# Kernel tuning notes

Measured on AMD Instinct MI355X. Metric: run time of the kernel, lower is better.

The kernel has to match this reference:

```python
import jax, jax.numpy as jnp
import numpy as np

N_NODES = 100000
HEADS = 4
NEG_SLOPE = 0.2


def setup_inputs() -> dict:
    key = jax.random.key(0)
    ks = jax.random.split(key, 16)
    in_dim, hidden, emb = 128, 64, 64
    hc = hidden // HEADS  # per-head channels layer1
    ec = emb // HEADS     # per-head channels layer2

    def glorot(k, shape):
        fan = shape[0] + shape[-1]
        lim = jnp.sqrt(6.0 / fan)
        return jax.random.uniform(k, shape, jnp.float32, -lim, lim)

    x = jax.random.normal(ks[0], (N_NODES, in_dim), jnp.float32)
    edge_index = jax.random.randint(ks[1], (2, 1600000), 0, N_NODES, jnp.int64)
    return {
        "x": x,
        "edge_index": edge_index,
        "W1": glorot(ks[2], (in_dim, hidden)),
        "a1_src": glorot(ks[3], (HEADS, hc)),
        "a1_dst": glorot(ks[4], (HEADS, hc)),
        "b1": jnp.zeros((hidden,), jnp.float32),
        "W2": glorot(ks[5], (hidden, emb)),
        "a2_src": glorot(ks[6], (HEADS, ec)),
        "a2_dst": glorot(ks[7], (HEADS, ec)),
        "b2": jnp.zeros((emb,), jnp.float32),
        "Wp": glorot(ks[8], (emb, emb)),
        "bp": jnp.zeros((emb,), jnp.float32),
    }


def gat_layer(x, src, dst, W, a_src, a_dst, b):
    """PyG GATConv (concat=True, add_self_loops already in src/dst, no dropout/eval)."""
    N = x.shape[0]
    H, C = a_src.shape
    xw = (x @ W).reshape(N, H, C)                       # [N,H,C]
    al_src = jnp.einsum('nhc,hc->nh', xw, a_src)        # [N,H]
    al_dst = jnp.einsum('nhc,hc->nh', xw, a_dst)
    e = al_src[src] + al_dst[dst]                       # [E,H]
    e = jnp.where(e > 0, e, NEG_SLOPE * e)              # leaky_relu
    # segment softmax over incoming edges of each destination node
    m = jax.ops.segment_max(e, dst, num_segments=N)     # [N,H]
    m = jnp.where(jnp.isfinite(m), m, 0.0)
    ee = jnp.exp(e - m[dst])
    s = jax.ops.segment_sum(ee, dst, num_segments=N)    # [N,H]
    alpha = ee / (s[dst] + 1e-16)                       # [E,H]
    msg = xw[src] * alpha[:, :, None]                   # [E,H,C]
    out = jax.ops.segment_sum(msg, dst, num_segments=N) # [N,H,C]
    return out.reshape(N, H * C) + b


def reference(x, edge_index, W1, a1_src, a1_dst, b1, W2, a2_src, a2_dst, b2, Wp, bp):
    N = x.shape[0]
    loops = jnp.arange(N, dtype=edge_index.dtype)
    src = jnp.concatenate([edge_index[0], loops])
    dst = jnp.concatenate([edge_index[1], loops])
    h = jax.nn.elu(gat_layer(x, src, dst, W1, a1_src, a1_dst, b1))
    h = gat_layer(h, src, dst, W2, a2_src, a2_dst, b2)
    return jax.nn.elu(h) @ Wp + bp
```

## Files before the change

### kernel.cpp

```cpp
#include <hip/hip_runtime.h>
#include <hip/hip_bf16.h>
#include <math.h>

#define NEG_SLOPE 0.2f
#define BCAP 6144
#define ECHUNK 8192

typedef __bf16 bf16x8 __attribute__((ext_vector_type(8)));
typedef float  f32x4  __attribute__((ext_vector_type(4)));

__device__ __forceinline__ unsigned short f2b(float f) {
    union { float f; unsigned u; } c; c.f = f;
    unsigned r = (c.u + 0x7fffu + ((c.u >> 16) & 1u)) >> 16;
    return (unsigned short)r;
}
__device__ __forceinline__ float b2f(unsigned short s) {
    union { unsigned u; float f; } c; c.u = ((unsigned)s) << 16;
    return c.f;
}

__global__ __launch_bounds__(256) void k_feat1(
    const float* __restrict__ x, const float* __restrict__ W1,
    const float* __restrict__ a_src, const float* __restrict__ a_dst,
    unsigned short* __restrict__ xwb, float* __restrict__ als, float* __restrict__ ald,
    int* __restrict__ bcur, int NB, int N)
{
    int t = threadIdx.x;
    int gid = blockIdx.x * 256 + t;
    if (gid < NB) bcur[gid] = 0;

    __shared__ unsigned short WT[64][136];
    for (int f = t; f < 128 * 64; f += 256) {
        int k = f >> 6, c = f & 63;
        WT[c][k] = f2b(W1[f]);
    }
    __syncthreads();
    int wave = t >> 6, lane = t & 63;
    int lrow = lane & 15, lgrp = lane >> 4;
    int r0 = blockIdx.x * 64 + wave * 16;
    if (r0 >= N) return;

    bf16x8 bf[4][4];
#pragma unroll
    for (int ct = 0; ct < 4; ++ct)
#pragma unroll
        for (int ks = 0; ks < 4; ++ks)
            bf[ct][ks] = *(const bf16x8*)&WT[ct * 16 + lrow][ks * 32 + lgrp * 8];

    f32x4 acc[4];
#pragma unroll
    for (int ct = 0; ct < 4; ++ct) acc[ct] = (f32x4){0.f, 0.f, 0.f, 0.f};

    int rowA = r0 + lrow; if (rowA >= N) rowA = N - 1;
    const float* xp = x + (size_t)rowA * 128 + lgrp * 8;
#pragma unroll
    for (int ks = 0; ks < 4; ++ks) {
        f32x4 v0 = *(const f32x4*)(xp + ks * 32);
        f32x4 v1 = *(const f32x4*)(xp + ks * 32 + 4);
        union { unsigned short s[8]; bf16x8 b; } af;
        af.s[0] = f2b(v0[0]); af.s[1] = f2b(v0[1]); af.s[2] = f2b(v0[2]); af.s[3] = f2b(v0[3]);
        af.s[4] = f2b(v1[0]); af.s[5] = f2b(v1[1]); af.s[6] = f2b(v1[2]); af.s[7] = f2b(v1[3]);
#pragma unroll
        for (int ct = 0; ct < 4; ++ct)
            acc[ct] = __builtin_amdgcn_mfma_f32_16x16x32_bf16(af.b, bf[ct][ks], acc[ct], 0, 0, 0);
    }

    float asv[4], adv[4];
#pragma unroll
    for (int ct = 0; ct < 4; ++ct) { asv[ct] = a_src[ct * 16 + lrow]; adv[ct] = a_dst[ct * 16 + lrow]; }
#pragma unroll
    for (int q = 0; q < 4; ++q) {
        int row = r0 + lgrp * 4 + q;
        bool ok = row < N;
#pragma unroll
        for (int ct = 0; ct < 4; ++ct) {
            float v = acc[ct][q];
            if (ok) xwb[(size_t)row * 64 + ct * 16 + lrow] = f2b(v);
            float ps = v * asv[ct], pd = v * adv[ct];
#pragma unroll
            for (int m = 1; m < 16; m <<= 1) {
                ps += __shfl_xor(ps, m, 64);
                pd += __shfl_xor(pd, m, 64);
            }
            if (ok && lrow == 0) { als[row * 4 + ct] = ps; ald[row * 4 + ct] = pd; }
        }
    }
}

__global__ __launch_bounds__(256) void k_feat2(
    const unsigned short* __restrict__ hb, const float* __restrict__ W,
    const float* __restrict__ a_src, const float* __restrict__ a_dst,
    unsigned short* __restrict__ xwb, float* __restrict__ als, float* __restrict__ ald, int N)
{
    __shared__ unsigned short WT[64][72];
    int t = threadIdx.x;
    for (int f = t; f < 64 * 64; f += 256) {
        int k = f >> 6, c = f & 63;
        WT[c][k] = f2b(W[f]);
    }
    __syncthreads();
    int wave = t >> 6, lane = t & 63;
    int lrow = lane & 15, lgrp = lane >> 4;
    int r0 = blockIdx.x * 64 + wave * 16;
    if (r0 >= N) return;

    bf16x8 bf[4][2];
#pragma unroll
    for (int ct = 0; ct < 4; ++ct)
#pragma unroll
        for (int ks = 0; ks < 2; ++ks)
            bf[ct][ks] = *(const bf16x8*)&WT[ct * 16 + lrow][ks * 32 + lgrp * 8];

    f32x4 acc[4];
#pragma unroll
    for (int ct = 0; ct < 4; ++ct) acc[ct] = (f32x4){0.f, 0.f, 0.f, 0.f};

    int rowA = r0 + lrow; if (rowA >= N) rowA = N - 1;
    const unsigned short* hp = hb + (size_t)rowA * 64 + lgrp * 8;
#pragma unroll
    for (int ks = 0; ks < 2; ++ks) {
        bf16x8 af = *(const bf16x8*)(hp + ks * 32);
#pragma unroll
        for (int ct = 0; ct < 4; ++ct)
            acc[ct] = __builtin_amdgcn_mfma_f32_16x16x32_bf16(af, bf[ct][ks], acc[ct], 0, 0, 0);
    }

    float asv[4], adv[4];
#pragma unroll
    for (int ct = 0; ct < 4; ++ct) { asv[ct] = a_src[ct * 16 + lrow]; adv[ct] = a_dst[ct * 16 + lrow]; }
#pragma unroll
    for (int q = 0; q < 4; ++q) {
        int row = r0 + lgrp * 4 + q;
        bool ok = row < N;
#pragma unroll
        for (int ct = 0; ct < 4; ++ct) {
            float v = acc[ct][q];
            if (ok) xwb[(size_t)row * 64 + ct * 16 + lrow] = f2b(v);
            float ps = v * asv[ct], pd = v * adv[ct];
#pragma unroll
            for (int m = 1; m < 16; m <<= 1) {
                ps += __shfl_xor(ps, m, 64);
                pd += __shfl_xor(pd, m, 64);
            }
            if (ok && lrow == 0) { als[row * 4 + ct] = ps; ald[row * 4 + ct] = pd; }
        }
    }
}

__global__ __launch_bounds__(256) void k_proj(
    const unsigned short* __restrict__ gb, const float* __restrict__ Wp,
    const float* __restrict__ bp, float* __restrict__ out, int N)
{
    __shared__ unsigned short WT[64][72];
    int t = threadIdx.x;
    for (int f = t; f < 64 * 64; f += 256) {
        int k = f >> 6, c = f & 63;
        WT[c][k] = f2b(Wp[f]);
    }
    __syncthreads();
    int wave = t >> 6, lane = t & 63;
    int lrow = lane & 15, lgrp = lane >> 4;
    int r0 = blockIdx.x * 64 + wave * 16;
    if (r0 >= N) return;

    bf16x8 bf[4][2];
#pragma unroll
    for (int ct = 0; ct < 4; ++ct)
#pragma unroll
        for (int ks = 0; ks < 2; ++ks)
            bf[ct][ks] = *(const bf16x8*)&WT[ct * 16 + lrow][ks * 32 + lgrp * 8];

    f32x4 acc[4];
#pragma unroll
    for (int ct = 0; ct < 4; ++ct) acc[ct] = (f32x4){0.f, 0.f, 0.f, 0.f};

    int rowA = r0 + lrow; if (rowA >= N) rowA = N - 1;
    const unsigned short* gp = gb + (size_t)rowA * 64 + lgrp * 8;
#pragma unroll
    for (int ks = 0; ks < 2; ++ks) {
        bf16x8 af = *(const bf16x8*)(gp + ks * 32);
#pragma unroll
        for (int ct = 0; ct < 4; ++ct)
            acc[ct] = __builtin_amdgcn_mfma_f32_16x16x32_bf16(af, bf[ct][ks], acc[ct], 0, 0, 0);
    }

    float bpv[4];
#pragma unroll
    for (int ct = 0; ct < 4; ++ct) bpv[ct] = bp[ct * 16 + lrow];
#pragma unroll
    for (int q = 0; q < 4; ++q) {
        int row = r0 + lgrp * 4 + q;
        if (row >= N) break;
#pragma unroll
        for (int ct = 0; ct < 4; ++ct)
            out[(size_t)row * 64 + ct * 16 + lrow] = acc[ct][q] + bpv[ct];
    }
}

__global__ __launch_bounds__(256) void k_bucket(const int* __restrict__ src, const int* __restrict__ dst,
                                                int* __restrict__ bcur, unsigned* __restrict__ bbuf,
                                                int E, int NB) {
    __shared__ int cnt[512];
    __shared__ int base[512];
    int t = threadIdx.x;
    int e0 = blockIdx.x * ECHUNK;
    int e1 = e0 + ECHUNK; if (e1 > E) e1 = E;
    for (int i = t; i < NB; i += 256) cnt[i] = 0;
    __syncthreads();
    for (int i = e0 + t; i < e1; i += 256) atomicAdd(&cnt[dst[i] >> 8], 1);
    __syncthreads();
    for (int i = t; i < NB; i += 256) {
        int c = cnt[i];
        base[i] = c ? atomicAdd(&bcur[i], c) : 0;
        cnt[i] = 0;
    }
    __syncthreads();
    for (int i = e0 + t; i < e1; i += 256) {
        int d = dst[i];
        int b = d >> 8;
        int rel = atomicAdd(&cnt[b], 1);
        int pos = base[b] + rel;
        if (pos < BCAP)
            bbuf[(size_t)b * BCAP + pos] = ((unsigned)src[i] << 8) | (unsigned)(d & 255);
    }
}

__global__ __launch_bounds__(512) void k_scanbases(const int* __restrict__ bcur, int* __restrict__ bbase,
                                                   int NB, int N) {
    __shared__ int ts[512];
    int t = threadIdx.x;
    int v = 0;
    if (t < NB) {
        int nb = bcur[t]; if (nb > BCAP) nb = BCAP;
        int vn = N - t * 256; if (vn > 256) vn = 256; if (vn < 0) vn = 0;
        v = nb + vn;
    }
    ts[t] = v;
    __syncthreads();
    for (int off = 1; off < 512; off <<= 1) {
        int u = (t >= off) ? ts[t - off] : 0;
        __syncthreads();
        ts[t] += u;
        __syncthreads();
    }
    if (t < NB) bbase[t] = ts[t] - v;
}

__global__ __launch_bounds__(256) void k_csr(const int* __restrict__ bcur, const unsigned* __restrict__ bbuf,
                                             const int* __restrict__ bbase,
                                             int* __restrict__ offs, int* __restrict__ ssrc, int N) {
    __shared__ unsigned ebuf[BCAP];
    __shared__ int cnt[256];
    __shared__ int scn[256];
    int t = threadIdx.x, b = blockIdx.x;
    int node = b * 256 + t;
    int nb = bcur[b]; if (nb > BCAP) nb = BCAP;
    const unsigned* bp = bbuf + (size_t)b * BCAP;
    cnt[t] = (node < N) ? 1 : 0;
    __syncthreads();
    for (int j = t; j < nb; j += 256) {
        unsigned v = bp[j];
        ebuf[j] = v;
        atomicAdd(&cnt[v & 255u], 1);
    }
    __syncthreads();
    int d = cnt[t];
    scn[t] = d;
    __syncthreads();
    for (int off = 1; off < 256; off <<= 1) {
        int u = (t >= off) ? scn[t - off] : 0;
        __syncthreads();
        scn[t] += u;
        __syncthreads();
    }
    int o = bbase[b] + scn[t] - d;
    if (node < N) {
        offs[node] = o;
        ssrc[o] = node;
        if (node == N - 1) offs[N] = o + d;
    }
    __syncthreads();
    cnt[t] = o + 1;
    __syncthreads();
    for (int j = t; j < nb; j += 256) {
        unsigned v = ebuf[j];
        int dl = v & 255u;
        int pos = atomicAdd(&cnt[dl], 1);
        ssrc[pos] = (int)(v >> 8);
    }
}

__global__ __launch_bounds__(256) void k_aggregate(
    const int* __restrict__ offs, const int* __restrict__ ssrc,
    const unsigned short* __restrict__ xwb, const float* __restrict__ alsrc,
    const float* __restrict__ aldst, const float* __restrict__ bias,
    unsigned short* __restrict__ hout, int N)
{
    __shared__ float wls[4][32 * 8];
    int t = threadIdx.x;
    int wave = t >> 6, lane = t & 63;
    int n = blockIdx.x * 4 + wave;
    if (n >= N) return;
    int half = lane >> 5;
    int cl = lane & 31;
    int hp = cl >> 3;
    int s0 = offs[n], s1 = offs[n + 1];
    f32x4 adv = *(const f32x4*)(aldst + (size_t)n * 4);
    float* wl = wls[wave];
    int* wli = (int*)wl;
    const char* xb = (const char*)xwb;
    float ssum = 0.f, acc0 = 0.f, acc1 = 0.f;

    for (int c0 = s0; c0 < s1; c0 += 32) {
        int nb = s1 - c0; if (nb > 32) nb = 32;
        if (lane < nb) {
            int s = ssrc[c0 + lane];
            f32x4 al = *(const f32x4*)(alsrc + (size_t)s * 4);
            int o8 = lane * 8;
            int ob = s << 7;
#pragma unroll
            for (int q = 0; q < 4; ++q) {
                float e = al[q] + adv[q];
                e = fmaxf(e, NEG_SLOPE * e);
                wl[o8 + 2 * q] = __expf(fminf(e, 60.f));
                wli[o8 + 2 * q + 1] = ob;
            }
        }
        int e = 0;
        for (; e + 8 <= nb; e += 8) {
#pragma unroll
            for (int u = 0; u < 4; ++u) {
                int idx = e + 2 * u + half;
                int bo = idx * 8 + hp * 2;
                float w = wl[bo];
                int   o = wli[bo + 1];
                unsigned pv = *(const unsigned*)(xb + o + cl * 4);
                union { unsigned u_; float f; } lo, hi;
                lo.u_ = pv << 16;
                hi.u_ = pv & 0xffff0000u;
                ssum += w;
                acc0 = fmaf(w, lo.f, acc0);
                acc1 = fmaf(w, hi.f, acc1);
            }
        }
        for (; e < nb; e += 2) {
            int idx = e + half;
            if (idx < nb) {
                int bo = idx * 8 + hp * 2;
                float w = wl[bo];
                int   o = wli[bo + 1];
                unsigned pv = *(const unsigned*)(xb + o + cl * 4);
                union { unsigned u_; float f; } lo, hi;
                lo.u_ = pv << 16;
                hi.u_ = pv & 0xffff0000u;
                ssum += w;
                acc0 = fmaf(w, lo.f, acc0);
                acc1 = fmaf(w, hi.f, acc1);
            }
        }
    }

    ssum += __shfl_xor(ssum, 32, 64);
    acc0 += __shfl_xor(acc0, 32, 64);
    acc1 += __shfl_xor(acc1, 32, 64);
    float inv = 1.f / ssum;
    float2 bv = *(const float2*)(bias + 2 * cl);
    float h0 = fmaf(acc0, inv, bv.x);
    float h1 = fmaf(acc1, inv, bv.y);
    h0 = h0 > 0.f ? h0 : expm1f(h0);
    h1 = h1 > 0.f ? h1 : expm1f(h1);
    if (!half) {
        union { unsigned short s2[2]; unsigned u; } st;
        st.s2[0] = f2b(h0); st.s2[1] = f2b(h1);
        *(unsigned*)((char*)hout + ((size_t)n * 64 + cl * 2) * 2) = st.u;
    }
}

extern "C" void kernel_launch(void* const* d_in, const int* in_sizes, int n_in,
                              void* d_out, int out_size, void* d_ws, size_t ws_size,
                              hipStream_t stream) {
    const float* x   = (const float*)d_in[0];
    const int*   ei  = (const int*)d_in[1];
    const float* W1  = (const float*)d_in[2];
    const float* a1s = (const float*)d_in[3];
    const float* a1d = (const float*)d_in[4];
    const float* b1  = (const float*)d_in[5];
    const float* W2  = (const float*)d_in[6];
    const float* a2s = (const float*)d_in[7];
    const float* a2d = (const float*)d_in[8];
    const float* b2  = (const float*)d_in[9];
    const float* Wp  = (const float*)d_in[10];
    const float* bp  = (const float*)d_in[11];
    float* out = (float*)d_out;

    const int N = in_sizes[0] / 128;
    const int E = in_sizes[1] / 2;
    const int Etot = E + N;
    const int NB = (N + 255) >> 8;
    const int* esrc = ei;
    const int* edst = ei + E;

    char* p = (char*)d_ws;
    auto alloc = [&](size_t bytes) {
        char* r = p;
        p += (bytes + 255) & ~(size_t)255;
        return (void*)r;
    };
    unsigned short* xw1b = (unsigned short*)alloc((size_t)N * 64 * 2);
    unsigned short* xw2b = (unsigned short*)alloc((size_t)N * 64 * 2);
    unsigned short* h1b  = (unsigned short*)alloc((size_t)N * 64 * 2);
    unsigned short* h2b  = (unsigned short*)alloc((size_t)N * 64 * 2);
    float* al1sv = (float*)alloc((size_t)N * 4 * 4);
    float* al1dv = (float*)alloc((size_t)N * 4 * 4);
    float* al2sv = (float*)alloc((size_t)N * 4 * 4);
    float* al2dv = (float*)alloc((size_t)N * 4 * 4);
    int*   offs  = (int*)alloc((size_t)(N + 1) * 4);
    int*   ssrc  = (int*)alloc((size_t)Etot * 4);
    int*   bcur  = (int*)alloc((size_t)NB * 4);
    int*   bbase = (int*)alloc((size_t)(NB + 1) * 4);
    unsigned* bbuf = (unsigned*)alloc((size_t)NB * BCAP * 4);
    (void)ws_size; (void)n_in; (void)out_size;

    dim3 blk(256);
    int gEchunk = (E + ECHUNK - 1) / ECHUNK;
    int gN4   = (N + 3) / 4;
    int gN64  = (N + 63) / 64;

    k_feat1<<<gN64, blk, 0, stream>>>(x, W1, a1s, a1d, xw1b, al1sv, al1dv, bcur, NB, N);
    k_bucket<<<gEchunk, blk, 0, stream>>>(esrc, edst, bcur, bbuf, E, NB);
    k_scanbases<<<1, 512, 0, stream>>>(bcur, bbase, NB, N);
    k_csr<<<NB, blk, 0, stream>>>(bcur, bbuf, bbase, offs, ssrc, N);
    k_aggregate<<<gN4, blk, 0, stream>>>(offs, ssrc, xw1b, al1sv, al1dv, b1, h1b, N);
    k_feat2<<<gN64, blk, 0, stream>>>(h1b, W2, a2s, a2d, xw2b, al2sv, al2dv, N);
    k_aggregate<<<gN4, blk, 0, stream>>>(offs, ssrc, xw2b, al2sv, al2dv, b2, h2b, N);
    k_proj<<<gN64, blk, 0, stream>>>(h2b, Wp, bp, out, N);
}
```

Measured before the change: 208.8 us.

## Fuse bucket-base scan into CSR kernel, register-cache dst, unroll aggregation

Removes the single-block scan kernel by having each CSR block reduce the capped bucket counts of preceding buckets itself, saving a launch and a serial dependency. The bucket kernel keeps dst values in registers between its two passes to avoid reloading them. The aggregation inner loop gains a 16-edge unrolled path for more memory-level parallelism. Redundant per-block prefix work and higher register pressure are the costs.

```diff
diff --git a/kernel.cpp b/kernel.cpp
--- a/kernel.cpp
+++ b/kernel.cpp
@@ -205,9 +205,16 @@
     int t = threadIdx.x;
     int e0 = blockIdx.x * ECHUNK;
     int e1 = e0 + ECHUNK; if (e1 > E) e1 = E;
+    int dreg[ECHUNK / 256];
     for (int i = t; i < NB; i += 256) cnt[i] = 0;
     __syncthreads();
-    for (int i = e0 + t; i < e1; i += 256) atomicAdd(&cnt[dst[i] >> 8], 1);
+#pragma unroll
+    for (int k = 0; k < ECHUNK / 256; ++k) {
+        int i = e0 + k * 256 + t;
+        int d = (i < e1) ? dst[i] : -1;
+        dreg[k] = d;
+        if (d >= 0) atomicAdd(&cnt[d >> 8], 1);
+    }
     __syncthreads();
     for (int i = t; i < NB; i += 256) {
         int c = cnt[i];
@@ -215,49 +222,46 @@
         cnt[i] = 0;
     }
     __syncthreads();
-    for (int i = e0 + t; i < e1; i += 256) {
-        int d = dst[i];
-        int b = d >> 8;
-        int rel = atomicAdd(&cnt[b], 1);
-        int pos = base[b] + rel;
-        if (pos < BCAP)
-            bbuf[(size_t)b * BCAP + pos] = ((unsigned)src[i] << 8) | (unsigned)(d & 255);
-    }
-}
-
-__global__ __launch_bounds__(512) void k_scanbases(const int* __restrict__ bcur, int* __restrict__ bbase,
-                                                   int NB, int N) {
-    __shared__ int ts[512];
-    int t = threadIdx.x;
-    int v = 0;
-    if (t < NB) {
-        int nb = bcur[t]; if (nb > BCAP) nb = BCAP;
-        int vn = N - t * 256; if (vn > 256) vn = 256; if (vn < 0) vn = 0;
-        v = nb + vn;
-    }
-    ts[t] = v;
-    __syncthreads();
-    for (int off = 1; off < 512; off <<= 1) {
-        int u = (t >= off) ? ts[t - off] : 0;
-        __syncthreads();
-        ts[t] += u;
-        __syncthreads();
-    }
-    if (t < NB) bbase[t] = ts[t] - v;
+#pragma unroll
+    for (int k = 0; k < ECHUNK / 256; ++k) {
+        int i = e0 + k * 256 + t;
+        int d = dreg[k];
+        if (d >= 0) {
+            int b = d >> 8;
+            int rel = atomicAdd(&cnt[b], 1);
+            int pos = base[b] + rel;
+            if (pos < BCAP)
+                bbuf[(size_t)b * BCAP + pos] = ((unsigned)src[i] << 8) | (unsigned)(d & 255);
+        }
+    }
 }
 
 __global__ __launch_bounds__(256) void k_csr(const int* __restrict__ bcur, const unsigned* __restrict__ bbuf,
-                                             const int* __restrict__ bbase,
                                              int* __restrict__ offs, int* __restrict__ ssrc, int N) {
     __shared__ unsigned ebuf[BCAP];
     __shared__ int cnt[256];
     __shared__ int scn[256];
+    __shared__ int sbase;
     int t = threadIdx.x, b = blockIdx.x;
     int node = b * 256 + t;
     int nb = bcur[b]; if (nb > BCAP) nb = BCAP;
     const unsigned* bp = bbuf + (size_t)b * BCAP;
+
+    int ps = 0;
+    for (int j = t; j < b; j += 256) {
+        int c = bcur[j]; if (c > BCAP) c = BCAP;
+        ps += c;
+    }
+    scn[t] = ps;
     cnt[t] = (node < N) ? 1 : 0;
     __syncthreads();
+    for (int off = 128; off > 0; off >>= 1) {
+        if (t < off) scn[t] += scn[t + off];
+        __syncthreads();
+    }
+    if (t == 0) sbase = scn[0] + b * 256;
+    __syncthreads();
+
     for (int j = t; j < nb; j += 256) {
         unsigned v = bp[j];
         ebuf[j] = v;
@@ -273,7 +277,7 @@
         scn[t] += u;
         __syncthreads();
     }
-    int o = bbase[b] + scn[t] - d;
+    int o = sbase + scn[t] - d;
     if (node < N) {
         offs[node] = o;
         ssrc[o] = node;
@@ -327,6 +331,22 @@
             }
         }
         int e = 0;
+        for (; e + 16 <= nb; e += 16) {
+#pragma unroll
+            for (int u = 0; u < 8; ++u) {
+                int idx = e + 2 * u + half;
+                int bo = idx * 8 + hp * 2;
+                float w = wl[bo];
+                int   o = wli[bo + 1];
+                unsigned pv = *(const unsigned*)(xb + o + cl * 4);
+                union { unsigned u_; float f; } lo, hi;
+                lo.u_ = pv << 16;
+                hi.u_ = pv & 0xffff0000u;
+                ssum += w;
+                acc0 = fmaf(w, lo.f, acc0);
+                acc1 = fmaf(w, hi.f, acc1);
+            }
+        }
         for (; e + 8 <= nb; e += 8) {
 #pragma unroll
             for (int u = 0; u < 4; ++u) {
@@ -417,7 +437,6 @@
     int*   offs  = (int*)alloc((size_t)(N + 1) * 4);
     int*   ssrc  = (int*)alloc((size_t)Etot * 4);
     int*   bcur  = (int*)alloc((size_t)NB * 4);
-    int*   bbase = (int*)alloc((size_t)(NB + 1) * 4);
     unsigned* bbuf = (unsigned*)alloc((size_t)NB * BCAP * 4);
     (void)ws_size; (void)n_in; (void)out_size;
 
@@ -428,8 +447,7 @@
 
     k_feat1<<<gN64, blk, 0, stream>>>(x, W1, a1s, a1d, xw1b, al1sv, al1dv, bcur, NB, N);
     k_bucket<<<gEchunk, blk, 0, stream>>>(esrc, edst, bcur, bbuf, E, NB);
-    k_scanbases<<<1, 512, 0, stream>>>(bcur, bbase, NB, N);
-    k_csr<<<NB, blk, 0, stream>>>(bcur, bbuf, bbase, offs, ssrc, N);
+    k_csr<<<NB, blk, 0, stream>>>(bcur, bbuf, offs, ssrc, N);
     k_aggregate<<<gN4, blk, 0, stream>>>(offs, ssrc, xw1b, al1sv, al1dv, b1, h1b, N);
     k_feat2<<<gN64, blk, 0, stream>>>(h1b, W2, a2s, a2d, xw2b, al2sv, al2dv, N);
     k_aggregate<<<gN4, blk, 0, stream>>>(offs, ssrc, xw2b, al2sv, al2dv, b2, h2b, N);
```

Result: faster. 198.5 us (median of 2 runs) (-4.9%).
